# Kernel optimization log

Measured on AMD Instinct MI355X. Metric: run time of the kernel, lower is better.

Reference implementation:

```python
import jax, jax.numpy as jnp
import numpy as np

CL = 256   # context_length (global in original code)
IL = 64    # inst_length (global in original code)
PC, CH1, CH2, CH3 = 64, 128, 256, 256
CK1, CK2, CK3 = 3, 3, 3
CS1, CS2, CS3 = 1, 2, 2
CP1, CP2, CP3 = 1, 1, 1
BCH1, BCH2, BCH3 = 64, 128, 256
F1, OUT = 1024, 2
B = 2048
C3_OUT = 64 * CH3            # 16384, per __init__ formula with CL-1=255
F1_IN = C3_OUT + BCH3        # 16640


def _conv1d(x, W, b, stride, pad):
    # x: [B, Cin, L], W: [Cout, Cin, K]
    y = jax.lax.conv_general_dilated(x, W, window_strides=(stride,),
                                     padding=[(pad, pad)],
                                     dimension_numbers=("NCH", "OIH", "NCH"))
    return y + b[None, :, None]


def setup_inputs() -> dict:
    key = jax.random.key(0)
    ks = jax.random.split(key, 20)
    s = lambda *sh: 1.0 / np.sqrt(np.prod(sh[1:]))
    def w(k, *sh):
        return jax.random.normal(k, sh, dtype=jnp.float32) * s(*sh)
    return {
        "x": jax.random.normal(ks[0], (B, CL * IL), dtype=jnp.float32),
        "Wp": w(ks[1], PC, IL, 2), "bp": jnp.zeros((PC,), jnp.float32),
        "W1": w(ks[2], CH1, PC, CK1), "b1": jnp.zeros((CH1,), jnp.float32),
        "W2": w(ks[3], CH2, CH1, CK2), "b2": jnp.zeros((CH2,), jnp.float32),
        "W3": w(ks[4], CH3, CH2, CK3), "b3": jnp.zeros((CH3,), jnp.float32),
        "Wb1": w(ks[5], BCH1, IL), "bb1": jnp.zeros((BCH1,), jnp.float32),
        "Wb2": w(ks[6], BCH2, BCH1), "bb2": jnp.zeros((BCH2,), jnp.float32),
        "Wb3": w(ks[7], BCH3, BCH2), "bb3": jnp.zeros((BCH3,), jnp.float32),
        "Wfc1": w(ks[8], F1, F1_IN), "bfc1": jnp.zeros((F1,), jnp.float32),
        "Wfc2": w(ks[9], OUT, F1), "bfc2": jnp.zeros((OUT,), jnp.float32),
    }


def reference(x, Wp, bp, W1, b1, W2, b2, W3, b3,
              Wb1, bb1, Wb2, bb2, Wb3, bb3, Wfc1, bfc1, Wfc2, bfc2):
    xr = x.reshape(-1, CL, IL).transpose(0, 2, 1)   # [B, IL, CL]
    x0 = xr[:, :, 0]                                 # [B, IL]
    # Fused replacement for the convp loop: kernel-2 conv over (x0, x_i)
    # y[:, :, i-1] = Wp[:,:,0] @ x0 + Wp[:,:,1] @ x_i + bp
    y = (jnp.einsum("bi,pi->bp", x0, Wp[:, :, 0])[:, :, None]
         + jnp.einsum("bic,pi->bpc", xr[:, :, 1:], Wp[:, :, 1])
         + bp[None, :, None])                        # [B, PC, CL-1]
    # bypass path on the first instruction (kernel-size-1 convs == matmuls)
    f = jax.nn.relu(x0 @ Wb1.T + bb1)
    f = jax.nn.relu(f @ Wb2.T + bb2)
    f = jax.nn.relu(f @ Wb3.T + bb3)                 # [B, BCH3]
    h = jax.nn.relu(y)
    h = jax.nn.relu(_conv1d(h, W1, b1, CS1, CP1))
    h = jax.nn.relu(_conv1d(h, W2, b2, CS2, CP2))
    h = jax.nn.relu(_conv1d(h, W3, b3, CS3, CP3))    # [B, CH3, 64]
    h = h.reshape(h.shape[0], C3_OUT)
    z = jnp.concatenate([h, f], axis=1)              # [B, F1_IN]
    z = jax.nn.relu(z @ Wfc1.T + bfc1)
    return z @ Wfc2.T + bfc2                         # [B, OUT]
```

## Files before the change

kernel.cpp:

```cpp
#include <hip/hip_runtime.h>
#include <cstdint>
#include <cstddef>

typedef __attribute__((ext_vector_type(8))) short bf16x8;
typedef __attribute__((ext_vector_type(8))) unsigned short ushort8;
typedef __attribute__((ext_vector_type(4))) float f32x4;

__device__ __forceinline__ unsigned short f2bf(float f){
  unsigned int u = __float_as_uint(f);
  unsigned int lsb = (u >> 16) & 1u;
  u += 0x7fffu + lsb;
  return (unsigned short)(u >> 16);
}

__global__ __launch_bounds__(256) void pack_w_bf16_kernel(const float* __restrict__ W,
    unsigned short* __restrict__ Wb, int COUT, int CIN){
  int idx = blockIdx.x*256 + threadIdx.x;
  int tot = COUT*CIN*3;
  if (idx >= tot) return;
  int o = idx/(CIN*3); int r = idx - o*(CIN*3); int kk = r/CIN; int ci = r - kk*CIN;
  Wb[idx] = f2bf(W[(o*CIN + ci)*3 + kk]);
}

__global__ __launch_bounds__(256) void pack_wp_kernel(const float* __restrict__ Wp,
                                                      unsigned short* __restrict__ Bw){
  int idx = blockIdx.x*256 + threadIdx.x;
  if (idx >= 64*128) return;
  int p = idx >> 7, k = idx & 127;
  float v = (k < 64) ? Wp[p*128 + k*2] : Wp[p*128 + (k-64)*2 + 1];
  Bw[idx] = f2bf(v);
}

__global__ __launch_bounds__(256) void f2bf_kernel(const float* __restrict__ src,
                                                   unsigned short* __restrict__ dst, int n){
  int i = blockIdx.x*256 + threadIdx.x;
  if (i < n) dst[i] = f2bf(src[i]);
}

__global__ __launch_bounds__(256) void zero_guards_kernel(unsigned short* __restrict__ buf,
                                                          int LINP, int CIN, int nb){
  int idx = blockIdx.x*256 + threadIdx.x;
  int per = 2*CIN/8;
  if (idx >= nb*per) return;
  int b = idx / per, r = idx - b*per;
  int g = r / (CIN/8), c8 = r - g*(CIN/8);
  ushort8 z = {0,0,0,0,0,0,0,0};
  *(ushort8*)(buf + ((size_t)b*LINP + (size_t)g*(LINP-1))*CIN + c8*8) = z;
}

__global__ __launch_bounds__(256) void branch_kernel(const float* __restrict__ x,
    const float* __restrict__ Wb1, const float* __restrict__ bb1,
    const float* __restrict__ Wb2, const float* __restrict__ bb2,
    const float* __restrict__ Wb3, const float* __restrict__ bb3,
    unsigned short* __restrict__ Hcat){
  __shared__ float s0[64], s1[64], s2[128];
  const int b = blockIdx.x, tid = threadIdx.x;
  const float* xb = x + (size_t)b*16384;
  if (tid < 64) s0[tid] = xb[tid];
  __syncthreads();
  if (tid < 64){
    float a = bb1[tid];
    for (int k=0;k<64;k++) a = fmaf(Wb1[tid*64+k], s0[k], a);
    s1[tid] = fmaxf(a, 0.f);
  }
  __syncthreads();
  if (tid < 128){
    float a = bb2[tid];
    for (int k=0;k<64;k++) a = fmaf(Wb2[tid*64+k], s1[k], a);
    s2[tid] = fmaxf(a, 0.f);
  }
  __syncthreads();
  float a = bb3[tid];
  for (int k=0;k<128;k++) a = fmaf(Wb3[tid*128+k], s2[k], a);
  Hcat[(size_t)b*16640 + 16384 + tid] = f2bf(fmaxf(a, 0.f));
}

__global__ __launch_bounds__(256) void h0_gemm_kernel(const float* __restrict__ x,
    const unsigned short* __restrict__ Bw, const float* __restrict__ bp,
    unsigned short* __restrict__ h0o){
  __shared__ __align__(16) char sAraw[128*256];
  __shared__ __align__(16) char sBraw[64*256];
  const int tid = threadIdx.x;
  const int m0 = blockIdx.x*128;
  #pragma unroll
  for (int i=0;i<16;i++){
    int j = tid + 256*i;
    int row = j >> 5, q = j & 31;
    int m = m0 + row;
    int b = m / 255, c = m - b*255;
    const float* xb = x + (size_t)b*16384;
    int k = q*4;
    const float* src = (k < 64) ? (xb + k) : (xb + (c+1)*64 + (k-64));
    float4 v = *(const float4*)src;
    ushort4 u; u.x=f2bf(v.x); u.y=f2bf(v.y); u.z=f2bf(v.z); u.w=f2bf(v.w);
    *(ushort4*)(sAraw + row*256 + ((k*2) ^ ((row&7)<<4))) = u;
  }
  #pragma unroll
  for (int i=0;i<4;i++){
    int j = tid + 256*i;
    int row = j >> 4, q = j & 15;
    int k = q*8;
    ushort8 u = *(const ushort8*)(Bw + row*128 + k);
    *(ushort8*)(sBraw + row*256 + ((k*2) ^ ((row&7)<<4))) = u;
  }
  __syncthreads();
  const int lane = tid & 63, wid = tid >> 6;
  const int lr = lane & 15, lg = lane >> 4;
  f32x4 acc[2][4];
  #pragma unroll
  for (int a=0;a<2;a++)
    #pragma unroll
    for (int j=0;j<4;j++) acc[a][j] = (f32x4){0,0,0,0};
  #pragma unroll
  for (int ks=0; ks<4; ks++){
    int k = ks*32 + lg*8;
    bf16x8 af[2], bfr[4];
    #pragma unroll
    for (int f=0; f<2; f++){
      int row = wid*32 + f*16 + lr;
      af[f] = *(const bf16x8*)(sAraw + row*256 + ((k*2) ^ ((row&7)<<4)));
    }
    #pragma unroll
    for (int f=0; f<4; f++){
      int row = f*16 + lr;
      bfr[f] = *(const bf16x8*)(sBraw + row*256 + ((k*2) ^ ((row&7)<<4)));
    }
    #pragma unroll
    for (int fi=0; fi<2; fi++)
      #pragma unroll
      for (int fj=0; fj<4; fj++)
        acc[fi][fj] = __builtin_amdgcn_mfma_f32_16x16x32_bf16(af[fi], bfr[fj], acc[fi][fj], 0,0,0);
  }
  #pragma unroll
  for (int fi=0; fi<2; fi++)
    #pragma unroll
    for (int fj=0; fj<4; fj++)
      #pragma unroll
      for (int j=0;j<4;j++){
        int m = m0 + wid*32 + fi*16 + lg*4 + j;
        int n = fj*16 + lr;
        int b = m / 255, t = m - b*255;
        h0o[((size_t)b*257 + t + 1)*64 + n] = f2bf(fmaxf(acc[fi][fj][j] + bp[n], 0.f));
      }
}

template<int CIN,int COUT,int S,int LINP,int LOUT,bool TO_HCAT>
__global__ __launch_bounds__(256) void conv_gemm_kernel(
    const unsigned short* __restrict__ in, const unsigned short* __restrict__ Wb,
    const float* __restrict__ bias, unsigned short* __restrict__ out){
  constexpr int K = 3*CIN;
  constexpr int KS = K/64;
  __shared__ __align__(16) char sA[2*128*128];
  __shared__ __align__(16) char sB[2*128*128];
  const int tid = threadIdx.x;
  int m0;
  {
    int bid = blockIdx.x, nwg = gridDim.x;
    if ((nwg & 7) == 0){ int q = nwg >> 3; m0 = ((bid & 7)*q + (bid >> 3))*128; }
    else m0 = bid*128;
  }
  const int n0 = blockIdx.y*128;
  const int lane = tid & 63, wid = tid >> 6;
  const int wm = wid >> 1, wn = wid & 1;
  const int lr = lane & 15, lg = lane >> 4;
  const int srow = lane >> 3;
  const int ch = lane & 7;
  const unsigned short* abase[4];
  const unsigned short* bbase[4];
  int dsto[4];
  #pragma unroll
  for (int s=0;s<4;s++){
    int row = wid*32 + s*8 + srow;
    int m = m0 + row;
    int b = m / LOUT, t = m - b*LOUT;
    abase[s] = in + ((size_t)b*LINP + (size_t)t*S)*CIN + ch*8;
    bbase[s] = Wb + (size_t)(n0+row)*K + ch*8;
    dsto[s] = row*128 + ((ch ^ srow) << 4);
  }
  f32x4 acc[4][4];
  #pragma unroll
  for (int i=0;i<4;i++)
    #pragma unroll
    for (int j=0;j<4;j++) acc[i][j] = (f32x4){0,0,0,0};

  ushort8 ra[4], rb[4];
  auto loadregs = [&](int ks){
    const int k0 = ks*64;
    #pragma unroll
    for (int s=0;s<4;s++){
      ra[s] = *(const ushort8*)(abase[s] + k0);
      rb[s] = *(const ushort8*)(bbase[s] + k0);
    }
  };
  auto writeregs = [&](int bufi){
    #pragma unroll
    for (int s=0;s<4;s++){
      *(ushort8*)(sA + bufi*16384 + dsto[s]) = ra[s];
      *(ushort8*)(sB + bufi*16384 + dsto[s]) = rb[s];
    }
  };
  loadregs(0); writeregs(0);
  if (KS > 1) loadregs(1);
  __syncthreads();
  int buf = 0;
  #pragma unroll
  for (int ks=0; ks<KS; ks++){
    #pragma unroll
    for (int kss=0; kss<2; kss++){
      const int k = kss*32 + lg*8;
      bf16x8 af[4], bfr[4];
      #pragma unroll
      for (int f=0;f<4;f++){
        int ra_ = wm*64 + f*16 + lr;
        af[f]  = *(const bf16x8*)(sA + buf*16384 + ra_*128 + ((k*2) ^ ((ra_&7)<<4)));
        int rb_ = wn*64 + f*16 + lr;
        bfr[f] = *(const bf16x8*)(sB + buf*16384 + rb_*128 + ((k*2) ^ ((rb_&7)<<4)));
      }
      #pragma unroll
      for (int fi=0;fi<4;fi++)
        #pragma unroll
        for (int fj=0;fj<4;fj++)
          acc[fi][fj] = __builtin_amdgcn_mfma_f32_16x16x32_bf16(af[fi], bfr[fj], acc[fi][fj], 0,0,0);
    }
    if (ks+1 < KS){
      writeregs(buf^1);
      if (ks+2 < KS) loadregs(ks+2);
    }
    __syncthreads();
    buf ^= 1;
  }
  #pragma unroll
  for (int fi=0;fi<4;fi++)
    #pragma unroll
    for (int fj=0;fj<4;fj++)
      #pragma unroll
      for (int j=0;j<4;j++){
        int m = m0 + wm*64 + fi*16 + lg*4 + j;
        int n = n0 + wn*64 + fj*16 + lr;
        int b = m / LOUT, t = m - b*LOUT;
        float val = fmaxf(acc[fi][fj][j] + bias[n], 0.f);
        if (TO_HCAT) out[(size_t)b*16640 + (size_t)n*64 + t] = f2bf(val);
        else         out[((size_t)b*(LOUT+2) + t + 1)*COUT + n] = f2bf(val);
      }
}

__global__ __launch_bounds__(256) void fc1_gemm_kernel(
    const unsigned short* __restrict__ A, const unsigned short* __restrict__ Bw,
    float* __restrict__ zp, int zoffm, int MT, int KZ){
  __shared__ __align__(16) char sA[2*128*128];
  __shared__ __align__(16) char sB[2*128*128];
  const int tid = threadIdx.x;
  const int nwg = gridDim.x;
  const int lgid = (blockIdx.x % 8)*(nwg/8) + blockIdx.x/8;
  const int kz  = lgid / (8*MT);
  const int rem = lgid % (8*MT);
  const int nt  = rem / MT;
  const int mt  = rem % MT;
  const int n0 = nt*128, m0 = mt*128;
  const int lane = tid & 63, wid = tid >> 6;
  const int wm = wid >> 1, wn = wid & 1;
  const int lr = lane & 15, lg = lane >> 4;
  const int srow = lane >> 3;
  const int ch = lane & 7;
  const unsigned short* abase[4];
  const unsigned short* bbase[4];
  int dsto[4];
  #pragma unroll
  for (int s=0;s<4;s++){
    int row = wid*32 + s*8 + srow;
    abase[s] = A  + (size_t)(m0+row)*16640 + ch*8;
    bbase[s] = Bw + (size_t)(n0+row)*16640 + ch*8;
    dsto[s] = row*128 + ((ch ^ srow) << 4);
  }
  f32x4 acc[4][4];
  #pragma unroll
  for (int i=0;i<4;i++)
    #pragma unroll
    for (int j=0;j<4;j++) acc[i][j] = (f32x4){0,0,0,0};
  const int it0 = (kz*260)/KZ, it1 = ((kz+1)*260)/KZ;

  ushort8 ra[4], rb[4];
  auto loadregs = [&](int it){
    const size_t k0 = (size_t)it*64;
    #pragma unroll
    for (int s=0;s<4;s++){
      ra[s] = *(const ushort8*)(abase[s] + k0);
      rb[s] = *(const ushort8*)(bbase[s] + k0);
    }
  };
  auto writeregs = [&](int bufi){
    #pragma unroll
    for (int s=0;s<4;s++){
      *(ushort8*)(sA + bufi*16384 + dsto[s]) = ra[s];
      *(ushort8*)(sB + bufi*16384 + dsto[s]) = rb[s];
    }
  };
  loadregs(it0); writeregs(0);
  if (it0+1 < it1) loadregs(it0+1);
  __syncthreads();
  int buf = 0;
  for (int it=it0; it<it1; ++it){
    #pragma unroll
    for (int ks=0; ks<2; ks++){
      const int k = ks*32 + lg*8;
      bf16x8 af[4], bfr[4];
      #pragma unroll
      for (int f=0;f<4;f++){
        int rowa = wm*64 + f*16 + lr;
        af[f]  = *(const bf16x8*)(sA + buf*16384 + rowa*128 + ((k*2) ^ ((rowa&7)<<4)));
        int rowb = wn*64 + f*16 + lr;
        bfr[f] = *(const bf16x8*)(sB + buf*16384 + rowb*128 + ((k*2) ^ ((rowb&7)<<4)));
      }
      #pragma unroll
      for (int fi=0;fi<4;fi++)
        #pragma unroll
        for (int fj=0;fj<4;fj++)
          acc[fi][fj] = __builtin_amdgcn_mfma_f32_16x16x32_bf16(af[fi], bfr[fj], acc[fi][fj], 0,0,0);
    }
    if (it+1 < it1){
      writeregs(buf^1);
      if (it+2 < it1) loadregs(it+2);
    }
    __syncthreads();
    buf ^= 1;
  }
  float* zo = zp + (size_t)kz*zoffm;
  #pragma unroll
  for (int fi=0;fi<4;fi++)
    #pragma unroll
    for (int fj=0;fj<4;fj++)
      #pragma unroll
      for (int j=0;j<4;j++){
        int m = m0 + wm*64 + fi*16 + lg*4 + j;
        int n = n0 + wn*64 + fj*16 + lr;
        zo[(size_t)m*1024 + n] = acc[fi][fj][j];
      }
}

__global__ __launch_bounds__(256) void fc2_kernel(const float* __restrict__ zp, int zoffm, int KZ,
    const float* __restrict__ bfc1, const float* __restrict__ Wfc2,
    const float* __restrict__ bfc2, float* __restrict__ out){
  __shared__ float red[4][2];
  const int b = blockIdx.x, tid = threadIdx.x;
  float a0 = 0.f, a1 = 0.f;
  for (int n = tid; n < 1024; n += 256){
    float s = bfc1[n];
    const float* zb = zp + (size_t)b*1024 + n;
    for (int kz = 0; kz < KZ; kz++) s += zb[(size_t)kz*zoffm];
    s = fmaxf(s, 0.f);
    a0 = fmaf(s, Wfc2[n], a0);
    a1 = fmaf(s, Wfc2[1024+n], a1);
  }
  #pragma unroll
  for (int m=32; m>=1; m>>=1){ a0 += __shfl_xor(a0, m, 64); a1 += __shfl_xor(a1, m, 64); }
  const int w = tid >> 6;
  if ((tid & 63) == 0){ red[w][0] = a0; red[w][1] = a1; }
  __syncthreads();
  if (tid == 0){
    out[(size_t)b*2]   = red[0][0]+red[1][0]+red[2][0]+red[3][0] + bfc2[0];
    out[(size_t)b*2+1] = red[0][1]+red[1][1]+red[2][1]+red[3][1] + bfc2[1];
  }
}

extern "C" void kernel_launch(void* const* d_in, const int* in_sizes, int n_in,
                              void* d_out, int out_size, void* d_ws, size_t ws_size,
                              hipStream_t stream){
  const float* x    = (const float*)d_in[0];
  const float* Wp   = (const float*)d_in[1];
  const float* bp   = (const float*)d_in[2];
  const float* W1   = (const float*)d_in[3];
  const float* b1   = (const float*)d_in[4];
  const float* W2   = (const float*)d_in[5];
  const float* b2   = (const float*)d_in[6];
  const float* W3   = (const float*)d_in[7];
  const float* b3   = (const float*)d_in[8];
  const float* Wb1  = (const float*)d_in[9];
  const float* bb1  = (const float*)d_in[10];
  const float* Wb2  = (const float*)d_in[11];
  const float* bb2  = (const float*)d_in[12];
  const float* Wb3  = (const float*)d_in[13];
  const float* bb3  = (const float*)d_in[14];
  const float* Wfc1 = (const float*)d_in[15];
  const float* bfc1 = (const float*)d_in[16];
  const float* Wfc2 = (const float*)d_in[17];
  const float* bfc2 = (const float*)d_in[18];
  float* out = (float*)d_out;

  size_t off = 0;
  char* basep = (char*)d_ws;
  auto carve = [&](size_t bytes)->char*{
    char* q = basep + off; off += (bytes + 255) & ~(size_t)255; return q;
  };
  unsigned short* W1b   = (unsigned short*)carve((size_t)128*3*64*2);
  unsigned short* W2b   = (unsigned short*)carve((size_t)256*3*128*2);
  unsigned short* W3b   = (unsigned short*)carve((size_t)256*3*256*2);
  unsigned short* Bwp   = (unsigned short*)carve((size_t)64*128*2);
  unsigned short* Wfc1b = (unsigned short*)carve((size_t)1024*16640*2);
  size_t fixed = off;

  int Bc = 128, KZ = 64;
  {
    const int bcs[5] = {2048, 1024, 512, 256, 128};
    const int kzs[5] = {4, 8, 16, 32, 64};
    for (int i = 0; i < 5; i++){
      size_t b = bcs[i];
      size_t need = fixed + b*((size_t)66560+65792+33280) + (size_t)kzs[i]*b*4096 + 16*256;
      if (need <= ws_size){ Bc = bcs[i]; KZ = kzs[i]; break; }
    }
  }
  const int NC = 2048/Bc;
  const int MT = Bc/128;
  unsigned short* buf1 = (unsigned short*)carve((size_t)Bc*66560);
  unsigned short* buf2 = (unsigned short*)carve((size_t)Bc*65792);
  unsigned short* Hcat = (unsigned short*)carve((size_t)Bc*33280);
  float*          zp   = (float*)carve((size_t)KZ*Bc*4096);
  const int zoffm = Bc*1024;

  hipLaunchKernelGGL(pack_w_bf16_kernel, dim3((128*64*3+255)/256), dim3(256), 0, stream, W1, W1b, 128, 64);
  hipLaunchKernelGGL(pack_w_bf16_kernel, dim3((256*128*3+255)/256), dim3(256), 0, stream, W2, W2b, 256, 128);
  hipLaunchKernelGGL(pack_w_bf16_kernel, dim3((256*256*3+255)/256), dim3(256), 0, stream, W3, W3b, 256, 256);
  hipLaunchKernelGGL(pack_wp_kernel, dim3(32), dim3(256), 0, stream, Wp, Bwp);
  hipLaunchKernelGGL(f2bf_kernel, dim3((17039360+255)/256), dim3(256), 0, stream, Wfc1, Wfc1b, 17039360);

  for (int c = 0; c < NC; ++c){
    const float* xc = x + (size_t)c*Bc*16384;
    hipLaunchKernelGGL(zero_guards_kernel, dim3((Bc*2*64/8+255)/256), dim3(256), 0, stream,
                       buf1, 257, 64, Bc);
    hipLaunchKernelGGL(zero_guards_kernel, dim3((Bc*2*128/8+255)/256), dim3(256), 0, stream,
                       buf2, 257, 128, Bc);
    hipLaunchKernelGGL(branch_kernel, dim3(Bc), dim3(256), 0, stream,
                       xc, Wb1, bb1, Wb2, bb2, Wb3, bb3, Hcat);
    hipLaunchKernelGGL(h0_gemm_kernel, dim3(Bc*255/128), dim3(256), 0, stream, xc, Bwp, bp, buf1);
    hipLaunchKernelGGL((conv_gemm_kernel<64,128,1,257,255,false>), dim3(Bc*255/128, 1), dim3(256), 0, stream,
                       buf1, W1b, b1, buf2);
    hipLaunchKernelGGL(zero_guards_kernel, dim3((Bc*2*256/8+255)/256), dim3(256), 0, stream,
                       buf1, 130, 256, Bc);
    hipLaunchKernelGGL((conv_gemm_kernel<128,256,2,257,128,false>), dim3(Bc, 2), dim3(256), 0, stream,
                       buf2, W2b, b2, buf1);
    hipLaunchKernelGGL((conv_gemm_kernel<256,256,2,130,64,true>), dim3(Bc/2, 2), dim3(256), 0, stream,
                       buf1, W3b, b3, Hcat);
    hipLaunchKernelGGL(fc1_gemm_kernel, dim3(8*MT*KZ), dim3(256), 0, stream,
                       Hcat, Wfc1b, zp, zoffm, MT, KZ);
    hipLaunchKernelGGL(fc2_kernel, dim3(Bc), dim3(256), 0, stream,
                       zp, zoffm, KZ, bfc1, Wfc2, bfc2, out + (size_t)c*Bc*2);
  }
}
```

Baseline: 547.3 us.

## Retile conv GEMMs to 512-thread blocks covering full output channels, single-buffered LDS

Rewrites the three conv GEMM launches to 512-thread workgroups whose tile spans all output channels (256x128 or 128x256), so each block loads the input rows once instead of once per N tile. The LDS double buffer is replaced by a single buffer with register prefetch and two barriers per k-step, and an M bound check handles the non-multiple tail for conv1. A global_load_lds helper is added but not used. The larger tiles reduce grid size and may lower occupancy, and the extra barrier can expose load latency.

Measured after the change: 742.6 us. +35.7%, slower.

```diff
diff --git a/kernel.cpp b/kernel.cpp
--- a/kernel.cpp
+++ b/kernel.cpp
@@ -11,6 +11,12 @@
   unsigned int lsb = (u >> 16) & 1u;
   u += 0x7fffu + lsb;
   return (unsigned short)(u >> 16);
+}
+
+__device__ __forceinline__ void gload16(const void* g, void* l){
+  __builtin_amdgcn_global_load_lds(
+      (const __attribute__((address_space(1))) unsigned int*)g,
+      (__attribute__((address_space(3))) unsigned int*)l, 16, 0, 0);
 }
 
 __global__ __launch_bounds__(256) void pack_w_bf16_kernel(const float* __restrict__ W,
@@ -144,38 +150,46 @@
       }
 }
 
-template<int CIN,int COUT,int S,int LINP,int LOUT,bool TO_HCAT>
-__global__ __launch_bounds__(256) void conv_gemm_kernel(
+template<int CIN,int COUT,int S,int LINP,int LOUT,int BM,int BN,int WM,int WN,bool TO_HCAT>
+__global__ __launch_bounds__(512, 4) void conv_gemm_kernel(
     const unsigned short* __restrict__ in, const unsigned short* __restrict__ Wb,
-    const float* __restrict__ bias, unsigned short* __restrict__ out){
+    const float* __restrict__ bias, unsigned short* __restrict__ out, int M){
   constexpr int K = 3*CIN;
   constexpr int KS = K/64;
-  __shared__ __align__(16) char sA[2*128*128];
-  __shared__ __align__(16) char sB[2*128*128];
+  constexpr int ALD = BM*8/512;
+  constexpr int BLD = BN*8/512;
+  __shared__ __align__(16) char sA[BM*128];
+  __shared__ __align__(16) char sB[BN*128];
   const int tid = threadIdx.x;
   int m0;
   {
     int bid = blockIdx.x, nwg = gridDim.x;
-    if ((nwg & 7) == 0){ int q = nwg >> 3; m0 = ((bid & 7)*q + (bid >> 3))*128; }
-    else m0 = bid*128;
-  }
-  const int n0 = blockIdx.y*128;
-  const int lane = tid & 63, wid = tid >> 6;
-  const int wm = wid >> 1, wn = wid & 1;
+    if ((nwg & 7) == 0){ int q = nwg >> 3; m0 = ((bid & 7)*q + (bid >> 3))*BM; }
+    else m0 = bid*BM;
+  }
+  const int lane = tid & 63, wv = tid >> 6;
+  const int wm = wv / WN, wn = wv % WN;
   const int lr = lane & 15, lg = lane >> 4;
-  const int srow = lane >> 3;
-  const int ch = lane & 7;
-  const unsigned short* abase[4];
-  const unsigned short* bbase[4];
-  int dsto[4];
-  #pragma unroll
-  for (int s=0;s<4;s++){
-    int row = wid*32 + s*8 + srow;
+
+  const unsigned short* abase[ALD];
+  const unsigned short* bbase[BLD];
+  int dstoA[ALD], dstoB[BLD];
+  #pragma unroll
+  for (int s=0;s<ALD;s++){
+    int slot = tid + s*512;
+    int row = slot >> 3, ch = slot & 7;
     int m = m0 + row;
+    if (m >= M) m = M-1;
     int b = m / LOUT, t = m - b*LOUT;
     abase[s] = in + ((size_t)b*LINP + (size_t)t*S)*CIN + ch*8;
-    bbase[s] = Wb + (size_t)(n0+row)*K + ch*8;
-    dsto[s] = row*128 + ((ch ^ srow) << 4);
+    dstoA[s] = row*128 + ((ch ^ (row&7)) << 4);
+  }
+  #pragma unroll
+  for (int s=0;s<BLD;s++){
+    int slot = tid + s*512;
+    int row = slot >> 3, ch = slot & 7;
+    bbase[s] = Wb + (size_t)row*K + ch*8;
+    dstoB[s] = row*128 + ((ch ^ (row&7)) << 4);
   }
   f32x4 acc[4][4];
   #pragma unroll
@@ -183,28 +197,26 @@
     #pragma unroll
     for (int j=0;j<4;j++) acc[i][j] = (f32x4){0,0,0,0};
 
-  ushort8 ra[4], rb[4];
+  ushort8 ra[ALD], rb[BLD];
   auto loadregs = [&](int ks){
     const int k0 = ks*64;
     #pragma unroll
-    for (int s=0;s<4;s++){
-      ra[s] = *(const ushort8*)(abase[s] + k0);
-      rb[s] = *(const ushort8*)(bbase[s] + k0);
-    }
+    for (int s=0;s<ALD;s++) ra[s] = *(const ushort8*)(abase[s] + k0);
+    #pragma unroll
+    for (int s=0;s<BLD;s++) rb[s] = *(const ushort8*)(bbase[s] + k0);
   };
-  auto writeregs = [&](int bufi){
-    #pragma unroll
-    for (int s=0;s<4;s++){
-      *(ushort8*)(sA + bufi*16384 + dsto[s]) = ra[s];
-      *(ushort8*)(sB + bufi*16384 + dsto[s]) = rb[s];
-    }
+  auto writeregs = [&](){
+    #pragma unroll
+    for (int s=0;s<ALD;s++) *(ushort8*)(sA + dstoA[s]) = ra[s];
+    #pragma unroll
+    for (int s=0;s<BLD;s++) *(ushort8*)(sB + dstoB[s]) = rb[s];
   };
-  loadregs(0); writeregs(0);
-  if (KS > 1) loadregs(1);
-  __syncthreads();
-  int buf = 0;
+  loadregs(0);
   #pragma unroll
   for (int ks=0; ks<KS; ks++){
+    writeregs();
+    if (ks+1 < KS) loadregs(ks+1);
+    __syncthreads();
     #pragma unroll
     for (int kss=0; kss<2; kss++){
       const int k = kss*32 + lg*8;
@@ -212,9 +224,9 @@
       #pragma unroll
       for (int f=0;f<4;f++){
         int ra_ = wm*64 + f*16 + lr;
-        af[f]  = *(const bf16x8*)(sA + buf*16384 + ra_*128 + ((k*2) ^ ((ra_&7)<<4)));
+        af[f]  = *(const bf16x8*)(sA + ra_*128 + ((k*2) ^ ((ra_&7)<<4)));
         int rb_ = wn*64 + f*16 + lr;
-        bfr[f] = *(const bf16x8*)(sB + buf*16384 + rb_*128 + ((k*2) ^ ((rb_&7)<<4)));
+        bfr[f] = *(const bf16x8*)(sB + rb_*128 + ((k*2) ^ ((rb_&7)<<4)));
       }
       #pragma unroll
       for (int fi=0;fi<4;fi++)
@@ -222,12 +234,7 @@
         for (int fj=0;fj<4;fj++)
           acc[fi][fj] = __builtin_amdgcn_mfma_f32_16x16x32_bf16(af[fi], bfr[fj], acc[fi][fj], 0,0,0);
     }
-    if (ks+1 < KS){
-      writeregs(buf^1);
-      if (ks+2 < KS) loadregs(ks+2);
-    }
     __syncthreads();
-    buf ^= 1;
   }
   #pragma unroll
   for (int fi=0;fi<4;fi++)
@@ -236,11 +243,13 @@
       #pragma unroll
       for (int j=0;j<4;j++){
         int m = m0 + wm*64 + fi*16 + lg*4 + j;
-        int n = n0 + wn*64 + fj*16 + lr;
-        int b = m / LOUT, t = m - b*LOUT;
-        float val = fmaxf(acc[fi][fj][j] + bias[n], 0.f);
-        if (TO_HCAT) out[(size_t)b*16640 + (size_t)n*64 + t] = f2bf(val);
-        else         out[((size_t)b*(LOUT+2) + t + 1)*COUT + n] = f2bf(val);
+        int n = wn*64 + fj*16 + lr;
+        if (m < M){
+          int b = m / LOUT, t = m - b*LOUT;
+          float val = fmaxf(acc[fi][fj][j] + bias[n], 0.f);
+          if (TO_HCAT) out[(size_t)b*16640 + (size_t)n*64 + t] = f2bf(val);
+          else         out[((size_t)b*(LOUT+2) + t + 1)*COUT + n] = f2bf(val);
+        }
       }
 }
 
@@ -431,14 +440,23 @@
     hipLaunchKernelGGL(branch_kernel, dim3(Bc), dim3(256), 0, stream,
                        xc, Wb1, bb1, Wb2, bb2, Wb3, bb3, Hcat);
     hipLaunchKernelGGL(h0_gemm_kernel, dim3(Bc*255/128), dim3(256), 0, stream, xc, Bwp, bp, buf1);
-    hipLaunchKernelGGL((conv_gemm_kernel<64,128,1,257,255,false>), dim3(Bc*255/128, 1), dim3(256), 0, stream,
-                       buf1, W1b, b1, buf2);
+    {
+      int M = Bc*255, gx = (M + 255)/256;
+      hipLaunchKernelGGL((conv_gemm_kernel<64,128,1,257,255,256,128,4,2,false>),
+                         dim3(gx), dim3(512), 0, stream, buf1, W1b, b1, buf2, M);
+    }
     hipLaunchKernelGGL(zero_guards_kernel, dim3((Bc*2*256/8+255)/256), dim3(256), 0, stream,
                        buf1, 130, 256, Bc);
-    hipLaunchKernelGGL((conv_gemm_kernel<128,256,2,257,128,false>), dim3(Bc, 2), dim3(256), 0, stream,
-                       buf2, W2b, b2, buf1);
-    hipLaunchKernelGGL((conv_gemm_kernel<256,256,2,130,64,true>), dim3(Bc/2, 2), dim3(256), 0, stream,
-                       buf1, W3b, b3, Hcat);
+    {
+      int M = Bc*128;
+      hipLaunchKernelGGL((conv_gemm_kernel<128,256,2,257,128,128,256,2,4,false>),
+                         dim3(M/128), dim3(512), 0, stream, buf2, W2b, b2, buf1, M);
+    }
+    {
+      int M = Bc*64;
+      hipLaunchKernelGGL((conv_gemm_kernel<256,256,2,130,64,128,256,2,4,true>),
+                         dim3(M/128), dim3(512), 0, stream, buf1, W3b, b3, Hcat, M);
+    }
     hipLaunchKernelGGL(fc1_gemm_kernel, dim3(8*MT*KZ), dim3(256), 0, stream,
                        Hcat, Wfc1b, zp, zoffm, MT, KZ);
     hipLaunchKernelGGL(fc2_kernel, dim3(Bc), dim3(256), 0, stream,
```
